# Kernel optimization log

Measured on AMD Instinct MI355X. Metric: run time of the kernel, lower is better.

The kernel has to match this reference:

```python
import jax, jax.numpy as jnp
import numpy as np

B = 1024
IN_SHAPE = ((8, 8, 8), (8, 8))
IN_RANKS = ((32, 32, 32), (32, 32))
OUT_SHAPE = (16, 16, 16)
OUT_RANK = (32, 32, 32)


def _xavier(key, shape):
    # xavier_normal over axes [0,1] (in) and [2] (out), matching the torch helper
    fan_in = shape[0] * shape[1]
    fan_out = shape[2]
    std = float(np.sqrt(2.0 / (fan_in + fan_out)))
    return jax.random.normal(key, shape, dtype=jnp.float32) * std


def setup_inputs() -> dict:
    key = jax.random.key(0)
    ks = jax.random.split(key, 12)
    x_dims = tuple(d for g in IN_SHAPE for d in g)
    inp = {"x": jax.random.normal(ks[0], (B,) + x_dims, dtype=jnp.float32)}
    # input TT factors, flattened over groups in order (group, mode)
    fac_shapes = []
    for shapes, ranks in zip(IN_SHAPE, IN_RANKS):
        for i in range(len(shapes)):
            r_prev = 1 if i == 0 else ranks[i - 1]
            fac_shapes.append((r_prev, shapes[i], ranks[i]))
    for idx, fs in enumerate(fac_shapes):
        inp[f"f{idx}"] = _xavier(ks[1 + idx], fs)
    # core: (last rank of each group..., output_rank[-1])
    core_shape = tuple(r[-1] for r in IN_RANKS) + (OUT_RANK[-1],)
    fan_in = int(np.prod(core_shape[:-1]))
    std = float(np.sqrt(2.0 / (fan_in + core_shape[-1])))
    inp["core"] = jax.random.normal(ks[6], core_shape, dtype=jnp.float32) * std
    # output TT factors
    for i in range(len(OUT_SHAPE)):
        r_prev = 1 if i == 0 else OUT_RANK[i - 1]
        inp[f"g{i}"] = _xavier(ks[7 + i], (r_prev, OUT_SHAPE[i], OUT_RANK[i]))
    # bias: uniform(-1/sqrt(fan_in), +) with fan_in = total input features
    total_in = int(np.prod([np.prod(s) for s in IN_SHAPE]))
    bound = 1.0 / float(np.sqrt(total_in))
    inp["bias"] = jax.random.uniform(ks[10], OUT_SHAPE, dtype=jnp.float32,
                                     minval=-bound, maxval=bound)
    return inp


def reference(x, f0, f1, f2, f3, f4, core, g0, g1, g2, bias):
    groups = ((f0, f1, f2), (f3, f4))
    Bsz = x.shape[0]
    # T: [B, remaining_modes_flat, accumulated_group_ranks_flat]
    T = x.reshape(Bsz, -1)[:, :, None]
    for facs in groups:
        first = facs[0][0]                       # squeeze dummy rank-1: [n, r]
        n = first.shape[0]
        T = T.reshape(Bsz, n, -1, T.shape[-1])   # [B, n, M', Racc]
        T = jnp.einsum("bnmq,nr->bmqr", T, first)  # [B, M', Racc, r]
        for f in facs[1:]:
            n = f.shape[1]
            T = T.reshape(Bsz, n, -1, T.shape[-2], T.shape[-1])
            T = jnp.einsum("bnmqp,pnr->bmqr", T, f)
        # fold this group's final rank into the accumulated rank axis
        T = T.reshape(Bsz, T.shape[1], -1)
    # all input modes consumed -> T is [B, 1, r1_last*r2_last]
    z = T.reshape(Bsz, -1) @ core.reshape(-1, core.shape[-1])  # [B, Rout]
    # output TT chain -> W[o0, o1, o2, R_last]
    W = g0[0]
    for g in (g1, g2):
        W = jnp.einsum("...p,poq->...oq", W, g)
    R = W.shape[-1]
    out = z @ W.reshape(-1, R).T                 # [B, prod(OUT_SHAPE)]
    out = out.reshape((Bsz,) + OUT_SHAPE)
    return out + bias
```

## Files before the change

kernel.cpp:

```cpp
#include <hip/hip_runtime.h>

#define WS_M2 0
#define WS_N2 16384
#define WS_WT 18432
#define WS_Z  149504

__global__ __launch_bounds__(256) void precompute_kernel(
    const float* __restrict__ f0, const float* __restrict__ f1,
    const float* __restrict__ f2, const float* __restrict__ f3,
    const float* __restrict__ f4, const float* __restrict__ g0,
    const float* __restrict__ g1, const float* __restrict__ g2,
    float* __restrict__ ws)
{
    __shared__ float sA[8192];
    const int t = threadIdx.x;
    const int blk = blockIdx.x;
    if (blk < 8) {
        for (int i = t; i < 2048; i += 256) {
            int a01 = i >> 5, r2 = i & 31;
            int a0 = a01 >> 3, a1 = a01 & 7;
            float s = 0.f;
            #pragma unroll
            for (int r1 = 0; r1 < 32; ++r1)
                s += f0[a0*32 + r1] * f1[r1*256 + a1*32 + r2];
            sA[i] = s;
        }
        __syncthreads();
        for (int i = t; i < 2048; i += 256) {
            int a012 = blk*64 + (i >> 5), r3 = i & 31;
            int a01 = a012 >> 3, a2 = a012 & 7;
            float s = 0.f;
            #pragma unroll
            for (int r2 = 0; r2 < 32; ++r2)
                s += sA[a01*32 + r2] * f2[r2*256 + a2*32 + r3];
            ws[WS_M2 + a012*32 + r3] = s;
        }
    } else if (blk == 8) {
        for (int i = t; i < 2048; i += 256) {
            int a34 = i >> 5, s2 = i & 31;
            int a3 = a34 >> 3, a4 = a34 & 7;
            float s = 0.f;
            #pragma unroll
            for (int s1 = 0; s1 < 32; ++s1)
                s += f3[a3*32 + s1] * f4[s1*256 + a4*32 + s2];
            ws[WS_N2 + i] = s;
        }
    } else {
        const int j = blk - 9;
        for (int i = t; i < 8192; i += 256) {
            int o01 = i >> 5, q = i & 31;
            int o0 = o01 >> 4, o1 = o01 & 15;
            float s = 0.f;
            #pragma unroll
            for (int p = 0; p < 32; ++p)
                s += g0[o0*32 + p] * g1[p*512 + o1*32 + q];
            sA[i] = s;
        }
        __syncthreads();
        for (int i = t; i < 4096; i += 256) {
            int o = j*128 + (i >> 5);
            int r = i & 31;
            int o01 = o >> 4, o2 = o & 15;
            float s = 0.f;
            #pragma unroll
            for (int q = 0; q < 32; ++q)
                s += sA[o01*32 + q] * g2[q*512 + o2*32 + r];
            ws[WS_WT + r*4096 + o] = s;
        }
    }
}

__global__ __launch_bounds__(256, 4) void main_kernel(
    const float* __restrict__ x, const float* __restrict__ core,
    const float* __restrict__ ws, float* __restrict__ zout)
{
    __shared__ float buf[8320];
    __shared__ float spart[512];
    const int t = threadIdx.x;
    const int b = blockIdx.x;
    const int w    = __builtin_amdgcn_readfirstlane(t >> 6);
    const int lane = t & 63;

    const float* __restrict__ xw = x + (size_t)b * 32768 + w * 8192 + lane;
    const float* __restrict__ m2 = ws + WS_M2 + w * 4096;

    float acc[32];
    #pragma unroll
    for (int r = 0; r < 32; ++r) acc[r] = 0.f;

    for (int k0 = 0; k0 < 128; k0 += 8) {
        float xv[8];
        #pragma unroll
        for (int i = 0; i < 8; ++i) xv[i] = xw[(k0 + i) * 64];
        #pragma unroll
        for (int i = 0; i < 8; ++i) {
            const float* __restrict__ mr = m2 + (k0 + i) * 32;
            #pragma unroll
            for (int r = 0; r < 32; ++r) acc[r] += xv[i] * mr[r];
        }
    }

    #pragma unroll
    for (int r = 0; r < 32; ++r) buf[w*2080 + r*65 + lane] = acc[r];
    __syncthreads();

    {
        const int rr = t >> 3;
        const int mb = (t & 7) * 8;
        float s[8];
        #pragma unroll
        for (int i = 0; i < 8; ++i) {
            s[i] = buf[rr*65 + mb + i] + buf[2080 + rr*65 + mb + i]
                 + buf[4160 + rr*65 + mb + i] + buf[6240 + rr*65 + mb + i];
        }
        #pragma unroll
        for (int i = 0; i < 8; ++i) buf[rr*65 + mb + i] = s[i];
    }
    __syncthreads();

    {
        const float4* n24 = (const float4*)(ws + WS_N2);
        float4* d = (float4*)(buf + 4160);
        d[t] = n24[t];
        d[256 + t] = n24[256 + t];
    }
    __syncthreads();

    {
        const int r3  = t >> 3;
        const int s2b = (t & 7) * 4;
        float a0=0.f, a1=0.f, a2=0.f, a3=0.f;
        #pragma unroll 8
        for (int m = 0; m < 64; ++m) {
            float av = buf[r3*65 + m];
            const float* n = &buf[4160 + m*32 + s2b];
            a0 += av*n[0]; a1 += av*n[1]; a2 += av*n[2]; a3 += av*n[3];
        }
        float* d = &buf[6240 + r3*32 + s2b];
        d[0]=a0; d[1]=a1; d[2]=a2; d[3]=a3;
    }
    __syncthreads();

    {
        const int ro2 = t & 15;
        const int kc  = t >> 4;
        const float2* core2 = (const float2*)core;
        float s0 = 0.f, s1 = 0.f;
        const int k0 = kc * 64;
        for (int k = k0; k < k0 + 64; ++k) {
            float tv = buf[6240 + k];
            float2 cv = core2[k*16 + ro2];
            s0 += tv*cv.x; s1 += tv*cv.y;
        }
        spart[kc*32 + ro2*2 + 0] = s0;
        spart[kc*32 + ro2*2 + 1] = s1;
    }
    __syncthreads();
    if (t < 32) {
        float s = 0.f;
        #pragma unroll
        for (int kc = 0; kc < 16; ++kc) s += spart[kc*32 + t];
        zout[b*32 + t] = s;
    }
}

__global__ __launch_bounds__(256) void out_kernel(
    const float* __restrict__ ws, const float* __restrict__ bias,
    float* __restrict__ out)
{
    __shared__ float sW[8192];
    __shared__ float sZt[2176];
    __shared__ float sB[256];
    const int t  = threadIdx.x;
    const int bt = blockIdx.x;
    const int ot = blockIdx.y;

    {
        const float4* wt4 = (const float4*)(ws + WS_WT);
        float4* d = (float4*)sW;
        #pragma unroll
        for (int i = 0; i < 8; ++i) {
            int idx = i*256 + t;
            int ro = idx >> 6, oc = idx & 63;
            d[idx] = wt4[ro*1024 + ot*64 + oc];
        }
    }
    {
        const float4* z4 = (const float4*)(ws + WS_Z) + bt*512;
        #pragma unroll
        for (int i = 0; i < 2; ++i) {
            int idx = i*256 + t;
            int bl = idx >> 3, r4 = idx & 7;
            float4 v = z4[idx];
            sZt[(r4*4 + 0)*68 + bl] = v.x;
            sZt[(r4*4 + 1)*68 + bl] = v.y;
            sZt[(r4*4 + 2)*68 + bl] = v.z;
            sZt[(r4*4 + 3)*68 + bl] = v.w;
        }
    }
    if (t < 64) {
        const float4* b4 = (const float4*)bias + ot*64;
        ((float4*)sB)[t] = b4[t];
    }
    __syncthreads();

    const int oc = t & 63;
    const int bg = t >> 6;
    const float4* sW4 = (const float4*)sW;
    const float4 bv = ((const float4*)sB)[oc];
    float4* out4 = (float4*)out;

    for (int bi = 0; bi < 16; bi += 4) {
        const int bl = bg*16 + bi;
        float4 a0 = bv, a1 = bv, a2 = bv, a3 = bv;
        #pragma unroll
        for (int ro = 0; ro < 32; ++ro) {
            float4 w = sW4[ro*64 + oc];
            float4 z = *(const float4*)&sZt[ro*68 + bl];
            a0.x += z.x*w.x; a0.y += z.x*w.y; a0.z += z.x*w.z; a0.w += z.x*w.w;
            a1.x += z.y*w.x; a1.y += z.y*w.y; a1.z += z.y*w.z; a1.w += z.y*w.w;
            a2.x += z.z*w.x; a2.y += z.z*w.y; a2.z += z.z*w.z; a2.w += z.z*w.w;
            a3.x += z.w*w.x; a3.y += z.w*w.y; a3.z += z.w*w.z; a3.w += z.w*w.w;
        }
        const size_t obase = (size_t)(bt*64 + bl) * 1024 + ot*64 + oc;
        out4[obase + 0*1024] = a0;
        out4[obase + 1*1024] = a1;
        out4[obase + 2*1024] = a2;
        out4[obase + 3*1024] = a3;
    }
}

extern "C" void kernel_launch(void* const* d_in, const int* in_sizes, int n_in,
                              void* d_out, int out_size, void* d_ws, size_t ws_size,
                              hipStream_t stream)
{
    const float* x    = (const float*)d_in[0];
    const float* f0   = (const float*)d_in[1];
    const float* f1   = (const float*)d_in[2];
    const float* f2   = (const float*)d_in[3];
    const float* f3   = (const float*)d_in[4];
    const float* f4   = (const float*)d_in[5];
    const float* core = (const float*)d_in[6];
    const float* g0   = (const float*)d_in[7];
    const float* g1   = (const float*)d_in[8];
    const float* g2   = (const float*)d_in[9];
    const float* bias = (const float*)d_in[10];
    float* ws  = (float*)d_ws;
    float* out = (float*)d_out;

    precompute_kernel<<<41, 256, 0, stream>>>(f0, f1, f2, f3, f4, g0, g1, g2, ws);
    main_kernel<<<1024, 256, 0, stream>>>(x, core, ws, ws + WS_Z);
    out_kernel<<<dim3(16, 16), 256, 0, stream>>>(ws, bias, out);
}
```

Baseline: 267.0 us.

## Stage x tiles into LDS via async global_load_lds with double buffering

The first contraction in main_kernel now copies x into shared memory with async global-to-LDS loads, double-buffered over 8 tiles so the next tile loads while the current one is computed. Work is split so each wave owns 8 of the 32 rank outputs across the full mode range, instead of each wave owning a quarter of the modes for all 32 ranks. That removes the cross-wave reduction pass and cuts accumulator registers from 32 to 8. In exchange each wave now reads all of x from LDS, and the loop adds a barrier per tile. The shared-memory footprint shrinks to one 32 KB buffer that is reused for the later stages.

Measured after the change: 357.9 us. +34.0%, slower.

```diff
diff --git a/kernel.cpp b/kernel.cpp
--- a/kernel.cpp
+++ b/kernel.cpp
@@ -1,9 +1,15 @@
 #include <hip/hip_runtime.h>
+#include <stdint.h>
 
 #define WS_M2 0
 #define WS_N2 16384
 #define WS_WT 18432
 #define WS_Z  149504
+
+#define GLOAD_LDS16(gsrc, ldst)                                         \
+    __builtin_amdgcn_global_load_lds(                                   \
+        (const __attribute__((address_space(1))) uint32_t*)(gsrc),      \
+        (__attribute__((address_space(3))) uint32_t*)(ldst), 16, 0, 0)
 
 __global__ __launch_bounds__(256) void precompute_kernel(
     const float* __restrict__ f0, const float* __restrict__ f1,
@@ -74,55 +80,59 @@
     const float* __restrict__ x, const float* __restrict__ core,
     const float* __restrict__ ws, float* __restrict__ zout)
 {
-    __shared__ float buf[8320];
-    __shared__ float spart[512];
+    __shared__ float xs[8192];
     const int t = threadIdx.x;
     const int b = blockIdx.x;
     const int w    = __builtin_amdgcn_readfirstlane(t >> 6);
     const int lane = t & 63;
 
-    const float* __restrict__ xw = x + (size_t)b * 32768 + w * 8192 + lane;
-    const float* __restrict__ m2 = ws + WS_M2 + w * 4096;
-
-    float acc[32];
+    const float* __restrict__ xb = x + (size_t)b * 32768;
+
+    {
+        const float* s = xb + w*1024 + lane*4;
+        float* d = xs + w*1024;
+        GLOAD_LDS16(s,       d);
+        GLOAD_LDS16(s + 256, d + 256);
+        GLOAD_LDS16(s + 512, d + 512);
+        GLOAD_LDS16(s + 768, d + 768);
+    }
+    __syncthreads();
+
+    float acc[8];
     #pragma unroll
-    for (int r = 0; r < 32; ++r) acc[r] = 0.f;
-
-    for (int k0 = 0; k0 < 128; k0 += 8) {
-        float xv[8];
-        #pragma unroll
-        for (int i = 0; i < 8; ++i) xv[i] = xw[(k0 + i) * 64];
-        #pragma unroll
-        for (int i = 0; i < 8; ++i) {
-            const float* __restrict__ mr = m2 + (k0 + i) * 32;
-            #pragma unroll
-            for (int r = 0; r < 32; ++r) acc[r] += xv[i] * mr[r];
-        }
+    for (int i = 0; i < 8; ++i) acc[i] = 0.f;
+
+    const float* __restrict__ m2w = ws + WS_M2 + w*8;
+
+    for (int tt = 0; tt < 8; ++tt) {
+        if (tt < 7) {
+            const float* s = xb + (tt+1)*4096 + w*1024 + lane*4;
+            float* d = xs + ((tt+1)&1)*4096 + w*1024;
+            GLOAD_LDS16(s,       d);
+            GLOAD_LDS16(s + 256, d + 256);
+            GLOAD_LDS16(s + 512, d + 512);
+            GLOAD_LDS16(s + 768, d + 768);
+        }
+        const float* __restrict__ xt  = xs + (tt&1)*4096;
+        const float* __restrict__ m2t = m2w + tt*2048;
+        #pragma unroll 8
+        for (int kk = 0; kk < 64; ++kk) {
+            float xv = xt[kk*64 + lane];
+            const float* __restrict__ mr = m2t + kk*32;
+            #pragma unroll
+            for (int i = 0; i < 8; ++i) acc[i] += xv * mr[i];
+        }
+        __syncthreads();
     }
 
     #pragma unroll
-    for (int r = 0; r < 32; ++r) buf[w*2080 + r*65 + lane] = acc[r];
-    __syncthreads();
-
-    {
-        const int rr = t >> 3;
-        const int mb = (t & 7) * 8;
-        float s[8];
-        #pragma unroll
-        for (int i = 0; i < 8; ++i) {
-            s[i] = buf[rr*65 + mb + i] + buf[2080 + rr*65 + mb + i]
-                 + buf[4160 + rr*65 + mb + i] + buf[6240 + rr*65 + mb + i];
-        }
-        #pragma unroll
-        for (int i = 0; i < 8; ++i) buf[rr*65 + mb + i] = s[i];
-    }
-    __syncthreads();
-
-    {
-        const float4* n24 = (const float4*)(ws + WS_N2);
-        float4* d = (float4*)(buf + 4160);
-        d[t] = n24[t];
-        d[256 + t] = n24[256 + t];
+    for (int i = 0; i < 8; ++i) xs[(w*8 + i)*65 + lane] = acc[i];
+
+    {
+        const float* s = ws + WS_N2 + w*512 + lane*4;
+        float* d = xs + 4096 + w*512;
+        GLOAD_LDS16(s,       d);
+        GLOAD_LDS16(s + 256, d + 256);
     }
     __syncthreads();
 
@@ -132,11 +142,11 @@
         float a0=0.f, a1=0.f, a2=0.f, a3=0.f;
         #pragma unroll 8
         for (int m = 0; m < 64; ++m) {
-            float av = buf[r3*65 + m];
-            const float* n = &buf[4160 + m*32 + s2b];
+            float av = xs[r3*65 + m];
+            const float* n = &xs[4096 + m*32 + s2b];
             a0 += av*n[0]; a1 += av*n[1]; a2 += av*n[2]; a3 += av*n[3];
         }
-        float* d = &buf[6240 + r3*32 + s2b];
+        float* d = &xs[6144 + r3*32 + s2b];
         d[0]=a0; d[1]=a1; d[2]=a2; d[3]=a3;
     }
     __syncthreads();
@@ -148,18 +158,18 @@
         float s0 = 0.f, s1 = 0.f;
         const int k0 = kc * 64;
         for (int k = k0; k < k0 + 64; ++k) {
-            float tv = buf[6240 + k];
+            float tv = xs[6144 + k];
             float2 cv = core2[k*16 + ro2];
             s0 += tv*cv.x; s1 += tv*cv.y;
         }
-        spart[kc*32 + ro2*2 + 0] = s0;
-        spart[kc*32 + ro2*2 + 1] = s1;
+        xs[7168 + kc*32 + ro2*2 + 0] = s0;
+        xs[7168 + kc*32 + ro2*2 + 1] = s1;
     }
     __syncthreads();
     if (t < 32) {
         float s = 0.f;
         #pragma unroll
-        for (int kc = 0; kc < 16; ++kc) s += spart[kc*32 + t];
+        for (int kc = 0; kc < 16; ++kc) s += xs[7168 + kc*32 + t];
         zout[b*32 + t] = s;
     }
 }
```

## Process four batch rows per block with M2 staged in LDS via direct loads

Applied to the files above, without the earlier changes.

The main kernel now handles four batch rows per 512-thread block. The 64KB M2 matrix and the N2 matrix are copied into LDS with global_load_lds, so M2 is read from global once per four batch rows instead of once per row. Each wave owns 4 of the 32 rank columns across all 512 x-rows, which removes the cross-wave partial-sum reduction. The cost is a large LDS footprint (about 107KB per block), which limits occupancy to a few blocks per CU, and only 256 blocks are launched.

Result: slower. 277.0 us (+3.7%).

```diff
diff --git a/kernel.cpp b/kernel.cpp
--- a/kernel.cpp
+++ b/kernel.cpp
@@ -1,9 +1,15 @@
 #include <hip/hip_runtime.h>
+#include <stdint.h>
 
 #define WS_M2 0
 #define WS_N2 16384
 #define WS_WT 18432
 #define WS_Z  149504
+
+#define GLOAD_LDS16(gsrc, ldst)                                         \
+    __builtin_amdgcn_global_load_lds(                                   \
+        (const __attribute__((address_space(1))) uint32_t*)(gsrc),      \
+        (__attribute__((address_space(3))) uint32_t*)(ldst), 16, 0, 0)
 
 __global__ __launch_bounds__(256) void precompute_kernel(
     const float* __restrict__ f0, const float* __restrict__ f1,
@@ -70,97 +76,115 @@
     }
 }
 
-__global__ __launch_bounds__(256, 4) void main_kernel(
+__global__ __launch_bounds__(512, 2) void main_kernel(
     const float* __restrict__ x, const float* __restrict__ core,
     const float* __restrict__ ws, float* __restrict__ zout)
 {
-    __shared__ float buf[8320];
-    __shared__ float spart[512];
+    __shared__ float s[26752];
     const int t = threadIdx.x;
-    const int b = blockIdx.x;
+    const int b0 = blockIdx.x * 4;
     const int w    = __builtin_amdgcn_readfirstlane(t >> 6);
     const int lane = t & 63;
 
-    const float* __restrict__ xw = x + (size_t)b * 32768 + w * 8192 + lane;
-    const float* __restrict__ m2 = ws + WS_M2 + w * 4096;
-
-    float acc[32];
+    {
+        const float* sm = ws + WS_M2 + w*2048 + lane*4;
+        float* dm = s + w*2048;
+        #pragma unroll
+        for (int i = 0; i < 8; ++i)
+            GLOAD_LDS16(sm + i*256, dm + i*256);
+        const float* sn = ws + WS_N2 + w*256 + lane*4;
+        GLOAD_LDS16(sn, s + 24704 + w*256);
+    }
+    __syncthreads();
+
+    float acc[4][4];
     #pragma unroll
-    for (int r = 0; r < 32; ++r) acc[r] = 0.f;
-
-    for (int k0 = 0; k0 < 128; k0 += 8) {
-        float xv[8];
-        #pragma unroll
-        for (int i = 0; i < 8; ++i) xv[i] = xw[(k0 + i) * 64];
+    for (int bb = 0; bb < 4; ++bb)
+        #pragma unroll
+        for (int rr = 0; rr < 4; ++rr) acc[bb][rr] = 0.f;
+
+    const float* xp0 = x + (size_t)(b0+0) * 32768 + lane;
+    const float* xp1 = x + (size_t)(b0+1) * 32768 + lane;
+    const float* xp2 = x + (size_t)(b0+2) * 32768 + lane;
+    const float* xp3 = x + (size_t)(b0+3) * 32768 + lane;
+    const float* mq  = s + w*4;
+
+    #pragma unroll 1
+    for (int k0 = 0; k0 < 512; k0 += 8) {
+        float xv[4][8];
         #pragma unroll
         for (int i = 0; i < 8; ++i) {
-            const float* __restrict__ mr = m2 + (k0 + i) * 32;
-            #pragma unroll
-            for (int r = 0; r < 32; ++r) acc[r] += xv[i] * mr[r];
+            xv[0][i] = xp0[i*64];
+            xv[1][i] = xp1[i*64];
+            xv[2][i] = xp2[i*64];
+            xv[3][i] = xp3[i*64];
+        }
+        xp0 += 512; xp1 += 512; xp2 += 512; xp3 += 512;
+        #pragma unroll
+        for (int i = 0; i < 8; ++i) {
+            float4 m4 = *(const float4*)(mq + (k0 + i)*32);
+            #pragma unroll
+            for (int bb = 0; bb < 4; ++bb) {
+                acc[bb][0] += xv[bb][i]*m4.x;
+                acc[bb][1] += xv[bb][i]*m4.y;
+                acc[bb][2] += xv[bb][i]*m4.z;
+                acc[bb][3] += xv[bb][i]*m4.w;
+            }
         }
     }
 
     #pragma unroll
-    for (int r = 0; r < 32; ++r) buf[w*2080 + r*65 + lane] = acc[r];
-    __syncthreads();
-
-    {
-        const int rr = t >> 3;
-        const int mb = (t & 7) * 8;
-        float s[8];
-        #pragma unroll
-        for (int i = 0; i < 8; ++i) {
-            s[i] = buf[rr*65 + mb + i] + buf[2080 + rr*65 + mb + i]
-                 + buf[4160 + rr*65 + mb + i] + buf[6240 + rr*65 + mb + i];
-        }
-        #pragma unroll
-        for (int i = 0; i < 8; ++i) buf[rr*65 + mb + i] = s[i];
-    }
-    __syncthreads();
-
-    {
-        const float4* n24 = (const float4*)(ws + WS_N2);
-        float4* d = (float4*)(buf + 4160);
-        d[t] = n24[t];
-        d[256 + t] = n24[256 + t];
-    }
-    __syncthreads();
-
-    {
-        const int r3  = t >> 3;
-        const int s2b = (t & 7) * 4;
-        float a0=0.f, a1=0.f, a2=0.f, a3=0.f;
+    for (int bb = 0; bb < 4; ++bb)
+        #pragma unroll
+        for (int rr = 0; rr < 4; ++rr)
+            s[16384 + bb*2080 + (w*4 + rr)*65 + lane] = acc[bb][rr];
+    __syncthreads();
+
+    {
+        const int bb  = t >> 7;
+        const int r3  = (t >> 2) & 31;
+        const int s2o = (t & 3) * 8;
+        float a[8];
+        #pragma unroll
+        for (int i = 0; i < 8; ++i) a[i] = 0.f;
+        const float* t3 = s + 16384 + bb*2080 + r3*65;
+        const float* n2 = s + 24704 + s2o;
         #pragma unroll 8
         for (int m = 0; m < 64; ++m) {
-            float av = buf[r3*65 + m];
-            const float* n = &buf[4160 + m*32 + s2b];
-            a0 += av*n[0]; a1 += av*n[1]; a2 += av*n[2]; a3 += av*n[3];
-        }
-        float* d = &buf[6240 + r3*32 + s2b];
-        d[0]=a0; d[1]=a1; d[2]=a2; d[3]=a3;
-    }
-    __syncthreads();
-
-    {
+            float av = t3[m];
+            const float* n = n2 + m*32;
+            #pragma unroll
+            for (int i = 0; i < 8; ++i) a[i] += av * n[i];
+        }
+        float* d = s + bb*1024 + r3*32 + s2o;
+        #pragma unroll
+        for (int i = 0; i < 8; ++i) d[i] = a[i];
+    }
+    __syncthreads();
+
+    {
+        const int bb  = t >> 7;
+        const int kc  = (t >> 4) & 7;
         const int ro2 = t & 15;
-        const int kc  = t >> 4;
         const float2* core2 = (const float2*)core;
         float s0 = 0.f, s1 = 0.f;
-        const int k0 = kc * 64;
-        for (int k = k0; k < k0 + 64; ++k) {
-            float tv = buf[6240 + k];
+        const int k0 = kc * 128;
+        for (int k = k0; k < k0 + 128; ++k) {
+            float tv = s[bb*1024 + k];
             float2 cv = core2[k*16 + ro2];
             s0 += tv*cv.x; s1 += tv*cv.y;
         }
-        spart[kc*32 + ro2*2 + 0] = s0;
-        spart[kc*32 + ro2*2 + 1] = s1;
-    }
-    __syncthreads();
-    if (t < 32) {
-        float s = 0.f;
-        #pragma unroll
-        for (int kc = 0; kc < 16; ++kc) s += spart[kc*32 + t];
-        zout[b*32 + t] = s;
+        s[4096 + bb*256 + kc*32 + ro2*2 + 0] = s0;
+        s[4096 + bb*256 + kc*32 + ro2*2 + 1] = s1;
+    }
+    __syncthreads();
+    if (t < 128) {
+        const int bb = t >> 5;
+        const int ro = t & 31;
+        float acc2 = 0.f;
+        #pragma unroll
+        for (int kc = 0; kc < 8; ++kc) acc2 += s[4096 + bb*256 + kc*32 + ro];
+        zout[(b0 + bb)*32 + ro] = acc2;
     }
 }
 
@@ -249,6 +273,6 @@
     float* out = (float*)d_out;
 
     precompute_kernel<<<41, 256, 0, stream>>>(f0, f1, f2, f3, f4, g0, g1, g2, ws);
-    main_kernel<<<1024, 256, 0, stream>>>(x, core, ws, ws + WS_Z);
+    main_kernel<<<256, 512, 0, stream>>>(x, core, ws, ws + WS_Z);
     out_kernel<<<dim3(16, 16), 256, 0, stream>>>(ws, bias, out);
 }
```

## Register-tile main contraction and stream M2 into LDS via async global_load_lds

Applied to the files above, without the earlier changes.

The first-stage contraction in main_kernel is restructured so each thread computes a 4x8 register tile, using float4 loads of x and of M2 rows from LDS. M2 chunks are double-buffered into LDS with global_load_lds, so each wave fetches its M2 slice once instead of every lane reading it from global/L1. LDS is merged into one buffer and the N2 load now overlaps the partial-sum reduction, which removes one barrier. Occupancy hint drops from 4 to 3 blocks per CU and LDS use grows, which may reduce latency hiding. Each wave reuses its own LDS buffer with only a vmcnt wait between chunks, so correctness depends on that wait ordering.

Measured after the change: 314.2 us. 17.7% more time.

```diff
diff --git a/kernel.cpp b/kernel.cpp
--- a/kernel.cpp
+++ b/kernel.cpp
@@ -1,9 +1,18 @@
 #include <hip/hip_runtime.h>
+#include <stdint.h>
 
 #define WS_M2 0
 #define WS_N2 16384
 #define WS_WT 18432
 #define WS_Z  149504
+
+#define GLOAD_LDS16(gsrc, ldst)                                         \
+    __builtin_amdgcn_global_load_lds(                                   \
+        (const __attribute__((address_space(1))) uint32_t*)(gsrc),      \
+        (__attribute__((address_space(3))) uint32_t*)(ldst), 16, 0, 0)
+
+#define FMA4(A, X, mm) do { (A).x += (X).x*(mm); (A).y += (X).y*(mm); \
+                            (A).z += (X).z*(mm); (A).w += (X).w*(mm); } while (0)
 
 __global__ __launch_bounds__(256) void precompute_kernel(
     const float* __restrict__ f0, const float* __restrict__ f1,
@@ -70,73 +79,101 @@
     }
 }
 
-__global__ __launch_bounds__(256, 4) void main_kernel(
+__global__ __launch_bounds__(256, 3) void main_kernel(
     const float* __restrict__ x, const float* __restrict__ core,
     const float* __restrict__ ws, float* __restrict__ zout)
 {
-    __shared__ float buf[8320];
-    __shared__ float spart[512];
+    __shared__ float s[12416];
     const int t = threadIdx.x;
     const int b = blockIdx.x;
     const int w    = __builtin_amdgcn_readfirstlane(t >> 6);
     const int lane = t & 63;
-
-    const float* __restrict__ xw = x + (size_t)b * 32768 + w * 8192 + lane;
-    const float* __restrict__ m2 = ws + WS_M2 + w * 4096;
-
-    float acc[32];
+    const int tm = lane & 7;
+    const int tr = lane >> 3;
+
+    const float* __restrict__ xq  = x + (size_t)b*32768 + w*8192 + tm*8;
+    const float* __restrict__ m2g = ws + WS_M2 + w*4096;
+    float* __restrict__ mbuf = s + w*1024;
+
+    GLOAD_LDS16(m2g + lane*4,       mbuf);
+    GLOAD_LDS16(m2g + 256 + lane*4, mbuf + 256);
+    asm volatile("s_waitcnt vmcnt(0)" ::: "memory");
+
+    float4 accA[4], accB[4];
     #pragma unroll
-    for (int r = 0; r < 32; ++r) acc[r] = 0.f;
-
-    for (int k0 = 0; k0 < 128; k0 += 8) {
-        float xv[8];
-        #pragma unroll
-        for (int i = 0; i < 8; ++i) xv[i] = xw[(k0 + i) * 64];
+    for (int rr = 0; rr < 4; ++rr) {
+        accA[rr].x = accA[rr].y = accA[rr].z = accA[rr].w = 0.f;
+        accB[rr].x = accB[rr].y = accB[rr].z = accB[rr].w = 0.f;
+    }
+
+    #pragma unroll 1
+    for (int c = 0; c < 8; ++c) {
+        if (c < 7) {
+            const float* sm = m2g + (c+1)*512 + lane*4;
+            float* dm = mbuf + ((c+1)&1)*512;
+            GLOAD_LDS16(sm,       dm);
+            GLOAD_LDS16(sm + 256, dm + 256);
+        }
+        const float* __restrict__ xc = xq + c*1024;
+        const float* __restrict__ mc = mbuf + (c&1)*512 + tr*4;
+        #pragma unroll 2
+        for (int kk = 0; kk < 16; ++kk) {
+            float4 xlo = *(const float4*)(xc + kk*64);
+            float4 xhi = *(const float4*)(xc + kk*64 + 4);
+            float4 m4  = *(const float4*)(mc + kk*32);
+            FMA4(accA[0], xlo, m4.x); FMA4(accB[0], xhi, m4.x);
+            FMA4(accA[1], xlo, m4.y); FMA4(accB[1], xhi, m4.y);
+            FMA4(accA[2], xlo, m4.z); FMA4(accB[2], xhi, m4.z);
+            FMA4(accA[3], xlo, m4.w); FMA4(accB[3], xhi, m4.w);
+        }
+        asm volatile("s_waitcnt vmcnt(0)" ::: "memory");
+    }
+
+    {
+        float* pw = s + 4096 + w*2080;
+        #pragma unroll
+        for (int rr = 0; rr < 4; ++rr) {
+            const int r = tr*4 + rr;
+            float* d = pw + r*65 + tm*8;
+            d[0]=accA[rr].x; d[1]=accA[rr].y; d[2]=accA[rr].z; d[3]=accA[rr].w;
+            d[4]=accB[rr].x; d[5]=accB[rr].y; d[6]=accB[rr].z; d[7]=accB[rr].w;
+        }
+    }
+    __syncthreads();
+
+    {
+        const float4* n24 = (const float4*)(ws + WS_N2);
+        float4* d = (float4*)s;
+        d[t]       = n24[t];
+        d[256 + t] = n24[256 + t];
+    }
+    {
+        float* P = s + 4096;
+        const int rr  = t >> 3;
+        const int mb2 = (t & 7) * 8;
+        float sum[8];
         #pragma unroll
         for (int i = 0; i < 8; ++i) {
-            const float* __restrict__ mr = m2 + (k0 + i) * 32;
-            #pragma unroll
-            for (int r = 0; r < 32; ++r) acc[r] += xv[i] * mr[r];
-        }
-    }
-
-    #pragma unroll
-    for (int r = 0; r < 32; ++r) buf[w*2080 + r*65 + lane] = acc[r];
-    __syncthreads();
-
-    {
-        const int rr = t >> 3;
-        const int mb = (t & 7) * 8;
-        float s[8];
-        #pragma unroll
-        for (int i = 0; i < 8; ++i) {
-            s[i] = buf[rr*65 + mb + i] + buf[2080 + rr*65 + mb + i]
-                 + buf[4160 + rr*65 + mb + i] + buf[6240 + rr*65 + mb + i];
-        }
-        #pragma unroll
-        for (int i = 0; i < 8; ++i) buf[rr*65 + mb + i] = s[i];
-    }
-    __syncthreads();
-
-    {
-        const float4* n24 = (const float4*)(ws + WS_N2);
-        float4* d = (float4*)(buf + 4160);
-        d[t] = n24[t];
-        d[256 + t] = n24[256 + t];
-    }
-    __syncthreads();
-
-    {
+            sum[i] = P[rr*65 + mb2 + i] + P[2080 + rr*65 + mb2 + i]
+                   + P[4160 + rr*65 + mb2 + i] + P[6240 + rr*65 + mb2 + i];
+        }
+        #pragma unroll
+        for (int i = 0; i < 8; ++i) P[rr*65 + mb2 + i] = sum[i];
+    }
+    __syncthreads();
+
+    {
+        const float* P = s + 4096;
         const int r3  = t >> 3;
         const int s2b = (t & 7) * 4;
         float a0=0.f, a1=0.f, a2=0.f, a3=0.f;
         #pragma unroll 8
         for (int m = 0; m < 64; ++m) {
-            float av = buf[r3*65 + m];
-            const float* n = &buf[4160 + m*32 + s2b];
+            float av = P[r3*65 + m];
+            const float* n = &s[m*32 + s2b];
             a0 += av*n[0]; a1 += av*n[1]; a2 += av*n[2]; a3 += av*n[3];
         }
-        float* d = &buf[6240 + r3*32 + s2b];
+        float* d = &s[2048 + r3*32 + s2b];
         d[0]=a0; d[1]=a1; d[2]=a2; d[3]=a3;
     }
     __syncthreads();
@@ -148,19 +185,19 @@
         float s0 = 0.f, s1 = 0.f;
         const int k0 = kc * 64;
         for (int k = k0; k < k0 + 64; ++k) {
-            float tv = buf[6240 + k];
+            float tv = s[2048 + k];
             float2 cv = core2[k*16 + ro2];
             s0 += tv*cv.x; s1 += tv*cv.y;
         }
-        spart[kc*32 + ro2*2 + 0] = s0;
-        spart[kc*32 + ro2*2 + 1] = s1;
+        s[3072 + kc*32 + ro2*2 + 0] = s0;
+        s[3072 + kc*32 + ro2*2 + 1] = s1;
     }
     __syncthreads();
     if (t < 32) {
-        float s = 0.f;
-        #pragma unroll
-        for (int kc = 0; kc < 16; ++kc) s += spart[kc*32 + t];
-        zout[b*32 + t] = s;
+        float acc = 0.f;
+        #pragma unroll
+        for (int kc = 0; kc < 16; ++kc) acc += s[3072 + kc*32 + t];
+        zout[b*32 + t] = acc;
     }
 }
 
```
